# Optimization experiments

Measured on AMD Instinct MI355X. Metric: run time of the kernel, lower is better.

Reference implementation:

```python
import jax, jax.numpy as jnp
import numpy as np

EPS = 1e-5

def setup_inputs() -> dict:
    key = jax.random.key(0)
    ks = jax.random.split(key, 4)
    B, C, H, W = 32, 256, 32, 32
    x = jax.random.normal(ks[0], (B, C, H, W), dtype=jnp.float32)
    gamma = jnp.ones((C,), dtype=jnp.float32)
    beta = jnp.zeros((C,), dtype=jnp.float32)
    # torch nn.Linear init scale ~ 1/sqrt(fan_in)
    W_kqv = jax.random.normal(ks[1], (3 * C, C), dtype=jnp.float32) / np.sqrt(C)
    b_kqv = jnp.zeros((3 * C,), dtype=jnp.float32)
    W_proj = jax.random.normal(ks[2], (C, C), dtype=jnp.float32) / np.sqrt(C)
    b_proj = jnp.zeros((C,), dtype=jnp.float32)
    return {"x": x, "gamma": gamma, "beta": beta, "W_kqv": W_kqv,
            "b_kqv": b_kqv, "W_proj": W_proj, "b_proj": b_proj}

def reference(x, gamma, beta, W_kqv, b_kqv, W_proj, b_proj):
    B, C, H, W = x.shape
    scale = jnp.sqrt(jnp.asarray(C, dtype=x.dtype))
    # BatchNorm2d (training-mode batch statistics, biased variance, eps=1e-5)
    mean = jnp.mean(x, axis=(0, 2, 3), keepdims=True)
    var = jnp.var(x, axis=(0, 2, 3), keepdims=True)
    t = (x - mean) * jax.lax.rsqrt(var + EPS)
    t = t * gamma[None, :, None, None] + beta[None, :, None, None]
    # [B, C, H, W] -> [B, N, C] with N = H*W
    t = t.reshape(B, C, H * W).transpose(0, 2, 1)
    kqv = t @ W_kqv.T + b_kqv           # [B, N, 3C]
    q, k, v = jnp.split(kqv, 3, axis=-1)  # each [B, N, C]
    s = jnp.einsum('bnc,bmc->bnm', q, k) / scale  # [B, N, N]
    attn = jax.nn.softmax(s, axis=-1)
    o = jnp.einsum('bnm,bmc->bnc', attn, v)        # [B, N, C]
    o = o @ W_proj.T + b_proj
    o = o.transpose(0, 2, 1).reshape(B, C, H, W)
    return o + x
```

## Files before the change

kernel.cpp:

```cpp
#include <hip/hip_runtime.h>

typedef unsigned short u16;
typedef __attribute__((ext_vector_type(8))) short bf16x8;
typedef __attribute__((ext_vector_type(4))) float f32x4;

__device__ __forceinline__ float bf2f(u16 u) {
  union { unsigned u; float f; } c; c.u = ((unsigned)u) << 16; return c.f;
}
__device__ __forceinline__ u16 f2bf(float f) {
  union { float f; unsigned u; } c; c.f = f;
  unsigned u = c.u;
  return (u16)((u + 0x7FFFu + ((u >> 16) & 1u)) >> 16);
}
__device__ __forceinline__ void gld16(const void* g, void* l) {
  __builtin_amdgcn_global_load_lds(
      (__attribute__((address_space(1))) void*)g,
      (__attribute__((address_space(3))) void*)l, 16, 0, 0);
}

#define SYNCB() do { \
  asm volatile("s_waitcnt vmcnt(0) lgkmcnt(0)" ::: "memory"); \
  __builtin_amdgcn_s_barrier(); \
  __builtin_amdgcn_sched_barrier(0); \
} while (0)

#define BB 32
#define CC 256
#define NN 1024

__global__ __launch_bounds__(256) void convert_w_kernel(
    const float* __restrict__ Wk, const float* __restrict__ bk,
    const float* __restrict__ Wp, const float* __restrict__ bp,
    u16* __restrict__ Wkb, u16* __restrict__ bkb,
    u16* __restrict__ Wpb, u16* __restrict__ bpb)
{
  int b = blockIdx.x, t = threadIdx.x;
  const float* src; u16* dst; int idx, n;
  if (b < 768)       { src = Wk; dst = Wkb; idx = b * 256 + t;        n = 196608; }
  else if (b < 771)  { src = bk; dst = bkb; idx = (b - 768) * 256 + t; n = 768;   }
  else if (b < 1027) { src = Wp; dst = Wpb; idx = (b - 771) * 256 + t; n = 65536; }
  else               { src = bp; dst = bpb; idx = t;                  n = 256;    }
  if (idx < n) dst[idx] = f2bf(src[idx]);
}

__global__ __launch_bounds__(256) void bn_stats_kernel(
    const float* __restrict__ x, const float* __restrict__ gamma,
    const float* __restrict__ beta, float* __restrict__ scl, float* __restrict__ sft)
{
  int c = blockIdx.x;
  int tid = threadIdx.x;
  float s = 0.f, q = 0.f;
  for (int g = tid; g < 8192; g += 256) {
    int b = g >> 8;
    int n = (g & 255) * 4;
    float4 v = *reinterpret_cast<const float4*>(x + (((size_t)(b * CC + c)) << 10) + n);
    s += v.x + v.y + v.z + v.w;
    q += v.x * v.x + v.y * v.y + v.z * v.z + v.w * v.w;
  }
  __shared__ float rs[256], rq[256];
  rs[tid] = s; rq[tid] = q;
  __syncthreads();
  for (int off = 128; off > 0; off >>= 1) {
    if (tid < off) { rs[tid] += rs[tid + off]; rq[tid] += rq[tid + off]; }
    __syncthreads();
  }
  if (tid == 0) {
    float mean = rs[0] * (1.f / 32768.f);
    float var  = rq[0] * (1.f / 32768.f) - mean * mean;
    float rstd = rsqrtf(var + 1e-5f);
    float g = gamma[c] * rstd;
    scl[c] = g;
    sft[c] = beta[c] - mean * g;
  }
}

__global__ __launch_bounds__(256, 2) void qkv_fused_kernel(
    const float* __restrict__ x, const float* __restrict__ scl,
    const float* __restrict__ sft, const u16* __restrict__ Wkb,
    const u16* __restrict__ bkb, u16* __restrict__ qkout, u16* __restrict__ vt)
{
  __shared__ __align__(16) u16 As[128 * 32];
  __shared__ __align__(16) u16 Bs[256 * 32];
  int bid = blockIdx.x;
  int bx = bid & 255, by = bid >> 8;
  int b = bx >> 3, nsp0 = (bx & 7) * 128;
  int tid = threadIdx.x, lane = tid & 63, w = tid >> 6;
  int lq = lane & 15, quad = lane >> 4;
  int wm = (w >> 1) * 64, wn = (w & 1) * 128;
  int ar = lane >> 2, ac = (lane & 3) * 8;
  int rbB = w * 64;
  int nn = tid & 127, ci0 = (tid >> 7) * 16;

  const float* xb = x + (((size_t)(b * CC)) << 10) + nsp0 + nn;
  const u16* Bw = Wkb + (size_t)(by * 256) * 256;

  f32x4 zero = {0.f, 0.f, 0.f, 0.f};
  f32x4 acc[4][8];
  #pragma unroll
  for (int i = 0; i < 4; ++i)
    #pragma unroll
    for (int j = 0; j < 8; ++j) acc[i][j] = zero;

  int swz = (nn >> 1) & 3;
  int jj0 = ci0 >> 3;

  for (int k0 = 0; k0 < 256; k0 += 32) {
    __syncthreads();
    #pragma unroll
    for (int i = 0; i < 4; ++i)
      gld16(Bw + (size_t)(rbB + i * 16 + ar) * 256 + k0 + ac,
            &Bs[(rbB + i * 16) * 32]);
    float sv[16], hv[16];
    #pragma unroll
    for (int g = 0; g < 4; ++g) {
      float4 a = *reinterpret_cast<const float4*>(scl + k0 + ci0 + g * 4);
      float4 d = *reinterpret_cast<const float4*>(sft + k0 + ci0 + g * 4);
      sv[g * 4 + 0] = a.x; sv[g * 4 + 1] = a.y; sv[g * 4 + 2] = a.z; sv[g * 4 + 3] = a.w;
      hv[g * 4 + 0] = d.x; hv[g * 4 + 1] = d.y; hv[g * 4 + 2] = d.z; hv[g * 4 + 3] = d.w;
    }
    u16 av[16];
    #pragma unroll
    for (int i = 0; i < 16; ++i) {
      float v = xb[((size_t)(k0 + ci0 + i)) << 10];
      av[i] = f2bf(v * sv[i] + hv[i]);
    }
    bf16x8 p0, p1;
    #pragma unroll
    for (int i = 0; i < 8; ++i) { p0[i] = (short)av[i]; p1[i] = (short)av[i + 8]; }
    *reinterpret_cast<bf16x8*>(&As[nn * 32 + ((jj0 ^ swz) << 3)]) = p0;
    *reinterpret_cast<bf16x8*>(&As[nn * 32 + (((jj0 + 1) ^ swz) << 3)]) = p1;
    __syncthreads();

    bf16x8 af[4], bfr[8];
    #pragma unroll
    for (int i = 0; i < 4; ++i) {
      int r = wm + i * 16 + lq;
      af[i] = *reinterpret_cast<const bf16x8*>(
          &As[r * 32 + ((quad ^ ((r >> 1) & 3)) << 3)]);
    }
    #pragma unroll
    for (int j = 0; j < 8; ++j)
      bfr[j] = *reinterpret_cast<const bf16x8*>(
          &Bs[(wn + j * 16 + lq) * 32 + quad * 8]);
    #pragma unroll
    for (int i = 0; i < 4; ++i)
      #pragma unroll
      for (int j = 0; j < 8; ++j)
        acc[i][j] = __builtin_amdgcn_mfma_f32_16x16x32_bf16(af[i], bfr[j], acc[i][j], 0, 0, 0);
  }

  if (by < 2) {
    #pragma unroll
    for (int j = 0; j < 8; ++j) {
      int col = by * 256 + wn + j * 16 + lq;
      float bv = bf2f(bkb[col]);
      #pragma unroll
      for (int i = 0; i < 4; ++i) {
        int m = (b << 10) + nsp0 + wm + i * 16 + quad * 4;
        #pragma unroll
        for (int r = 0; r < 4; ++r)
          qkout[(size_t)(m + r) * 512 + col] = f2bf(acc[i][j][r] + bv);
      }
    }
  } else {
    #pragma unroll
    for (int j = 0; j < 8; ++j) {
      int col = wn + j * 16 + lq;
      float bv = bf2f(bkb[512 + col]);
      #pragma unroll
      for (int i = 0; i < 4; ++i) {
        int n = nsp0 + wm + i * 16 + quad * 4;
        ushort4 o;
        o.x = f2bf(acc[i][j][0] + bv);
        o.y = f2bf(acc[i][j][1] + bv);
        o.z = f2bf(acc[i][j][2] + bv);
        o.w = f2bf(acc[i][j][3] + bv);
        *reinterpret_cast<ushort4*>(&vt[(size_t)b * 262144 + (size_t)col * 1024 + n]) = o;
      }
    }
  }
}

__global__ __launch_bounds__(256) void gemm_nt_kernel(
    const u16* __restrict__ A, int lda, size_t sA,
    const u16* __restrict__ B, int ldb, size_t sB,
    u16* __restrict__ C, int ldc, size_t sC,
    int K, const u16* __restrict__ bias, float scale, int mode,
    const float* __restrict__ xres, float* __restrict__ outf)
{
  __shared__ u16 As[128 * 32];
  __shared__ u16 Bs[128 * 32];
  int tid = threadIdx.x;
  int m0 = blockIdx.x * 128, n0 = blockIdx.y * 128;
  const u16* Ab = A + (size_t)blockIdx.z * sA;
  const u16* Bb = B + (size_t)blockIdx.z * sB;
  u16* Cb = C + (size_t)blockIdx.z * sC;

  int lane = tid & 63, w = tid >> 6;
  int lq = lane & 15, quad = lane >> 4;
  int wm = (w >> 1) * 64, wn = (w & 1) * 64;
  int ar = lane >> 2, ac = (lane & 3) * 8;
  int rb = w * 32;

  f32x4 zero = {0.f, 0.f, 0.f, 0.f};
  f32x4 acc[4][4];
  #pragma unroll
  for (int i = 0; i < 4; ++i)
    #pragma unroll
    for (int j = 0; j < 4; ++j) acc[i][j] = zero;

  for (int k0 = 0; k0 < K; k0 += 32) {
    __syncthreads();
    gld16(Ab + (size_t)(m0 + rb +      ar) * lda + k0 + ac, &As[(rb     ) * 32]);
    gld16(Ab + (size_t)(m0 + rb + 16 + ar) * lda + k0 + ac, &As[(rb + 16) * 32]);
    gld16(Bb + (size_t)(n0 + rb +      ar) * ldb + k0 + ac, &Bs[(rb     ) * 32]);
    gld16(Bb + (size_t)(n0 + rb + 16 + ar) * ldb + k0 + ac, &Bs[(rb + 16) * 32]);
    __syncthreads();
    bf16x8 af[4], bfr[4];
    #pragma unroll
    for (int i = 0; i < 4; ++i) {
      af[i]  = *reinterpret_cast<const bf16x8*>(&As[(wm + i * 16 + lq) * 32 + quad * 8]);
      bfr[i] = *reinterpret_cast<const bf16x8*>(&Bs[(wn + i * 16 + lq) * 32 + quad * 8]);
    }
    #pragma unroll
    for (int i = 0; i < 4; ++i)
      #pragma unroll
      for (int j = 0; j < 4; ++j)
        acc[i][j] = __builtin_amdgcn_mfma_f32_16x16x32_bf16(af[i], bfr[j], acc[i][j], 0, 0, 0);
  }

  #pragma unroll
  for (int j = 0; j < 4; ++j) {
    int col = n0 + wn + j * 16 + lq;
    float bv = bias ? bf2f(bias[col]) : 0.f;
    #pragma unroll
    for (int i = 0; i < 4; ++i) {
      int rbase = m0 + wm + i * 16 + quad * 4;
      if (mode == 2) {
        int b = rbase >> 10, n = rbase & 1023;
        size_t idx = (((size_t)(b * CC + col)) << 10) + n;
        float4 xv = *reinterpret_cast<const float4*>(xres + idx);
        float4 o;
        o.x = acc[i][j][0] * scale + bv + xv.x;
        o.y = acc[i][j][1] * scale + bv + xv.y;
        o.z = acc[i][j][2] * scale + bv + xv.z;
        o.w = acc[i][j][3] * scale + bv + xv.w;
        *reinterpret_cast<float4*>(outf + idx) = o;
      } else {
        #pragma unroll
        for (int r = 0; r < 4; ++r)
          Cb[(size_t)(rbase + r) * ldc + col] = f2bf(acc[i][j][r] * scale + bv);
      }
    }
  }
}

__global__ __launch_bounds__(512, 2) void attn_kernel(
    const u16* __restrict__ qk,
    const u16* __restrict__ vt,
    u16* __restrict__ o)
{
  __shared__ __align__(16) u16 Ks[2][64 * 256];
  __shared__ __align__(16) u16 Vs[2][256 * 64];
  __shared__ __align__(16) u16 Ps[128 * 64];
  float* rs = (float*)Ps;

  int bid = blockIdx.x;
  int b  = (bid & 7) + 8 * ((bid >> 3) & 3);
  int qt = bid >> 5;
  int tid = threadIdx.x, lane = tid & 63, w = tid >> 6;
  int lq = lane & 15, hh = lane >> 4;
  int wr = w & 3;
  bool isQK = w < 4;

  const u16* qb = qk + ((size_t)b << 10) * 512;
  const u16* kb = qb + 256;
  const u16* vb = vt + ((size_t)b << 18);

  auto stageK = [&](int kt, int bufi) {
    #pragma unroll
    for (int i = 0; i < 4; ++i) {
      int slot = i * 512 + tid;
      int r = slot >> 5, c = slot & 31;
      gld16(kb + (size_t)(kt * 64 + r) * 512 + ((c ^ (r & 7)) << 3),
            &Ks[bufi][(i * 512 + (tid & 448)) * 8]);
    }
  };
  auto stageV = [&](int kt, int bufi) {
    #pragma unroll
    for (int i = 0; i < 4; ++i) {
      int slot = i * 512 + tid;
      int n = slot >> 3, c = slot & 7;
      gld16(vb + (size_t)(n << 10) + kt * 64 + ((c ^ (n & 7)) << 3),
            &Vs[bufi][(i * 512 + (tid & 448)) * 8]);
    }
  };

  f32x4 zero = {0.f, 0.f, 0.f, 0.f};

  stageK(0, 0);
  SYNCB();

  if (isQK) {
    int q0 = qt * 128 + wr * 32;
    bf16x8 qf[2][8];
    #pragma unroll
    for (int qi = 0; qi < 2; ++qi)
      #pragma unroll
      for (int kk = 0; kk < 8; ++kk)
        qf[qi][kk] = *reinterpret_cast<const bf16x8*>(
            qb + (size_t)(q0 + qi * 16 + lq) * 512 + kk * 32 + hh * 8);
    float runsum[2][4] = {{0.f, 0.f, 0.f, 0.f}, {0.f, 0.f, 0.f, 0.f}};

    #pragma unroll 1
    for (int p = 0; p <= 16; ++p) {
      if (p <= 15) stageV(p, p & 1);
      if (p <= 14) stageK(p + 1, (p + 1) & 1);
      u16 pbv[2][4][4];
      if (p <= 15) {
        const u16* Kc = Ks[p & 1];
        f32x4 sacc[2][4];
        #pragma unroll
        for (int qi = 0; qi < 2; ++qi)
          #pragma unroll
          for (int ni = 0; ni < 4; ++ni) sacc[qi][ni] = zero;
        #pragma unroll
        for (int kk = 0; kk < 8; ++kk) {
          bf16x8 kf[4];
          #pragma unroll
          for (int ni = 0; ni < 4; ++ni) {
            int r = ni * 16 + lq;
            kf[ni] = *reinterpret_cast<const bf16x8*>(
                &Kc[r * 256 + (((kk * 4 + hh) ^ (r & 7)) << 3)]);
          }
          __builtin_amdgcn_s_setprio(1);
          #pragma unroll
          for (int qi = 0; qi < 2; ++qi)
            #pragma unroll
            for (int ni = 0; ni < 4; ++ni)
              sacc[qi][ni] = __builtin_amdgcn_mfma_f32_16x16x32_bf16(
                  qf[qi][kk], kf[ni], sacc[qi][ni], 0, 0, 0);
          __builtin_amdgcn_s_setprio(0);
        }
        #pragma unroll
        for (int qi = 0; qi < 2; ++qi)
          #pragma unroll
          for (int ni = 0; ni < 4; ++ni)
            #pragma unroll
            for (int rr = 0; rr < 4; ++rr) {
              float pexp = __expf(sacc[qi][ni][rr] * 0.0625f);
              u16 pb = f2bf(pexp);
              runsum[qi][rr] += bf2f(pb);
              pbv[qi][ni][rr] = pb;
            }
      }
      SYNCB();
      if (p <= 15) {
        #pragma unroll
        for (int qi = 0; qi < 2; ++qi)
          #pragma unroll
          for (int ni = 0; ni < 4; ++ni)
            #pragma unroll
            for (int rr = 0; rr < 4; ++rr) {
              int q = wr * 32 + qi * 16 + hh * 4 + rr;
              int kcol = ni * 16 + lq;
              Ps[q * 64 + ((((kcol >> 3) ^ (q & 7)) << 3) | (kcol & 7))] =
                  pbv[qi][ni][rr];
            }
      }
      SYNCB();
    }

    #pragma unroll
    for (int qi = 0; qi < 2; ++qi)
      #pragma unroll
      for (int rr = 0; rr < 4; ++rr) {
        float s = runsum[qi][rr];
        s += __shfl_xor(s, 1, 64);
        s += __shfl_xor(s, 2, 64);
        s += __shfl_xor(s, 4, 64);
        s += __shfl_xor(s, 8, 64);
        if (lq == 0) rs[wr * 32 + qi * 16 + hh * 4 + rr] = 1.f / s;
      }
    SYNCB();
  } else {
    f32x4 oacc[8][4];
    #pragma unroll
    for (int qi = 0; qi < 8; ++qi)
      #pragma unroll
      for (int nj = 0; nj < 4; ++nj) oacc[qi][nj] = zero;

    #pragma unroll 1
    for (int p = 0; p <= 16; ++p) {
      if (p <= 15) stageV(p, p & 1);
      if (p <= 14) stageK(p + 1, (p + 1) & 1);
      if (p >= 1) {
        const u16* Vc = Vs[(p - 1) & 1];
        #pragma unroll
        for (int kk2 = 0; kk2 < 2; ++kk2) {
          bf16x8 pa[8];
          #pragma unroll
          for (int qi = 0; qi < 8; ++qi) {
            int r = qi * 16 + lq;
            pa[qi] = *reinterpret_cast<const bf16x8*>(
                &Ps[r * 64 + (((kk2 * 4 + hh) ^ (r & 7)) << 3)]);
          }
          bf16x8 vf[4];
          #pragma unroll
          for (int nj = 0; nj < 4; ++nj) {
            int n = wr * 64 + nj * 16 + lq;
            vf[nj] = *reinterpret_cast<const bf16x8*>(
                &Vc[n * 64 + (((kk2 * 4 + hh) ^ (n & 7)) << 3)]);
          }
          __builtin_amdgcn_s_setprio(1);
          #pragma unroll
          for (int qi = 0; qi < 8; ++qi)
            #pragma unroll
            for (int nj = 0; nj < 4; ++nj)
              oacc[qi][nj] = __builtin_amdgcn_mfma_f32_16x16x32_bf16(
                  pa[qi], vf[nj], oacc[qi][nj], 0, 0, 0);
          __builtin_amdgcn_s_setprio(0);
        }
      }
      SYNCB();
      SYNCB();
    }

    SYNCB();
    float rinv[8][4];
    #pragma unroll
    for (int qi = 0; qi < 8; ++qi)
      #pragma unroll
      for (int rr = 0; rr < 4; ++rr)
        rinv[qi][rr] = rs[qi * 16 + hh * 4 + rr];
    u16* ob = o + ((size_t)(b << 10) + qt * 128) * 256;
    #pragma unroll
    for (int qi = 0; qi < 8; ++qi)
      #pragma unroll
      for (int nj = 0; nj < 4; ++nj)
        #pragma unroll
        for (int rr = 0; rr < 4; ++rr)
          ob[(size_t)(qi * 16 + hh * 4 + rr) * 256 + wr * 64 + nj * 16 + lq] =
              f2bf(oacc[qi][nj][rr] * rinv[qi][rr]);
  }
}

extern "C" void kernel_launch(void* const* d_in, const int* in_sizes, int n_in,
                              void* d_out, int out_size, void* d_ws, size_t ws_size,
                              hipStream_t stream) {
  const float* x     = (const float*)d_in[0];
  const float* gamma = (const float*)d_in[1];
  const float* beta  = (const float*)d_in[2];
  const float* Wkqv  = (const float*)d_in[3];
  const float* bkqv  = (const float*)d_in[4];
  const float* Wproj = (const float*)d_in[5];
  const float* bproj = (const float*)d_in[6];
  float* out = (float*)d_out;

  char* ws = (char*)d_ws;
  float* scl    = (float*)ws;
  float* sft    = (float*)(ws + 1024);
  u16* Wkb = (u16*)(ws + 4096);
  u16* bkb = Wkb + 196608;
  u16* Wpb = bkb + 768;
  u16* bpb = Wpb + 65536;
  u16* qk   = (u16*)(ws + 1048576);
  u16* vt   = qk + (size_t)32768 * 512;
  u16* o_pv = vt + (size_t)32 * 256 * 1024;

  convert_w_kernel<<<dim3(1028), dim3(256), 0, stream>>>(
      Wkqv, bkqv, Wproj, bproj, Wkb, bkb, Wpb, bpb);
  bn_stats_kernel<<<dim3(256), dim3(256), 0, stream>>>(x, gamma, beta, scl, sft);
  qkv_fused_kernel<<<dim3(768), dim3(256), 0, stream>>>(
      x, scl, sft, Wkb, bkb, qk, vt);
  attn_kernel<<<dim3(256), dim3(512), 0, stream>>>(qk, vt, o_pv);
  gemm_nt_kernel<<<dim3(256, 2, 1), dim3(256), 0, stream>>>(
      o_pv, 256, 0, Wpb, 256, 0, nullptr, 0, 0, 256, bpb, 1.0f, 2, x, out);
}
```

Baseline: 203.8 us.

## Double-buffer QKV GEMM tiles and prefetch next x slice in registers

The fused BN+QKV projection kernel now double-buffers the A and B LDS tiles. It issues the global loads for the next K-slice (weights via global_load_lds, x values into registers) before the current slice's MFMAs, so memory latency overlaps compute. The BN scale/shift vectors are staged once in shared memory instead of being reloaded from global memory each iteration. MFMA sections are raised in priority with s_setprio. Per-block LDS and register usage go up, which could lower occupancy, and the hand-written vmcnt(20) wait count has to match the number of loads actually in flight.

After: 197.4 us. 1.03x faster.

```diff
diff --git a/kernel.cpp b/kernel.cpp
--- a/kernel.cpp
+++ b/kernel.cpp
@@ -79,8 +79,9 @@
     const float* __restrict__ sft, const u16* __restrict__ Wkb,
     const u16* __restrict__ bkb, u16* __restrict__ qkout, u16* __restrict__ vt)
 {
-  __shared__ __align__(16) u16 As[128 * 32];
-  __shared__ __align__(16) u16 Bs[256 * 32];
+  __shared__ __align__(16) u16 As[2][128 * 32];
+  __shared__ __align__(16) u16 Bs[2][256 * 32];
+  __shared__ __align__(16) float SS[512];
   int bid = blockIdx.x;
   int bx = bid & 255, by = bid >> 8;
   int b = bx >> 3, nsp0 = (bx & 7) * 128;
@@ -104,49 +105,87 @@
   int swz = (nn >> 1) & 3;
   int jj0 = ci0 >> 3;
 
-  for (int k0 = 0; k0 < 256; k0 += 32) {
-    __syncthreads();
-    #pragma unroll
-    for (int i = 0; i < 4; ++i)
-      gld16(Bw + (size_t)(rbB + i * 16 + ar) * 256 + k0 + ac,
-            &Bs[(rbB + i * 16) * 32]);
+  if (tid < 128) {
+    const float* src = (tid < 64) ? (scl + tid * 4) : (sft + (tid - 64) * 4);
+    float4 v = *reinterpret_cast<const float4*>(src);
+    *reinterpret_cast<float4*>(&SS[(tid < 64) ? tid * 4 : 256 + (tid - 64) * 4]) = v;
+  }
+  __syncthreads();
+
+  float xA[16], xB[16];
+  #pragma unroll
+  for (int i = 0; i < 4; ++i)
+    gld16(Bw + (size_t)(rbB + i * 16 + ar) * 256 + ac, &Bs[0][(rbB + i * 16) * 32]);
+  #pragma unroll
+  for (int i = 0; i < 16; ++i)
+    xA[i] = xb[((size_t)(ci0 + i)) << 10];
+
+  auto body = [&](int t, float (&xc)[16], float (&xn)[16]) {
+    int k0 = t * 32;
+    if (t < 7) {
+      int kn = k0 + 32;
+      #pragma unroll
+      for (int i = 0; i < 4; ++i)
+        gld16(Bw + (size_t)(rbB + i * 16 + ar) * 256 + kn + ac,
+              &Bs[(t + 1) & 1][(rbB + i * 16) * 32]);
+      #pragma unroll
+      for (int i = 0; i < 16; ++i)
+        xn[i] = xb[((size_t)(kn + ci0 + i)) << 10];
+    }
     float sv[16], hv[16];
     #pragma unroll
     for (int g = 0; g < 4; ++g) {
-      float4 a = *reinterpret_cast<const float4*>(scl + k0 + ci0 + g * 4);
-      float4 d = *reinterpret_cast<const float4*>(sft + k0 + ci0 + g * 4);
-      sv[g * 4 + 0] = a.x; sv[g * 4 + 1] = a.y; sv[g * 4 + 2] = a.z; sv[g * 4 + 3] = a.w;
-      hv[g * 4 + 0] = d.x; hv[g * 4 + 1] = d.y; hv[g * 4 + 2] = d.z; hv[g * 4 + 3] = d.w;
-    }
+      f32x4 a = *reinterpret_cast<const f32x4*>(&SS[k0 + ci0 + g * 4]);
+      f32x4 d = *reinterpret_cast<const f32x4*>(&SS[256 + k0 + ci0 + g * 4]);
+      sv[g * 4 + 0] = a[0]; sv[g * 4 + 1] = a[1]; sv[g * 4 + 2] = a[2]; sv[g * 4 + 3] = a[3];
+      hv[g * 4 + 0] = d[0]; hv[g * 4 + 1] = d[1]; hv[g * 4 + 2] = d[2]; hv[g * 4 + 3] = d[3];
+    }
+    if (t < 7) {
+      asm volatile("s_waitcnt vmcnt(20)" ::: "memory");
+    } else {
+      asm volatile("s_waitcnt vmcnt(0)" ::: "memory");
+    }
+    __builtin_amdgcn_sched_barrier(0);
     u16 av[16];
     #pragma unroll
-    for (int i = 0; i < 16; ++i) {
-      float v = xb[((size_t)(k0 + ci0 + i)) << 10];
-      av[i] = f2bf(v * sv[i] + hv[i]);
-    }
+    for (int i = 0; i < 16; ++i)
+      av[i] = f2bf(xc[i] * sv[i] + hv[i]);
     bf16x8 p0, p1;
     #pragma unroll
     for (int i = 0; i < 8; ++i) { p0[i] = (short)av[i]; p1[i] = (short)av[i + 8]; }
-    *reinterpret_cast<bf16x8*>(&As[nn * 32 + ((jj0 ^ swz) << 3)]) = p0;
-    *reinterpret_cast<bf16x8*>(&As[nn * 32 + (((jj0 + 1) ^ swz) << 3)]) = p1;
-    __syncthreads();
+    *reinterpret_cast<bf16x8*>(&As[t & 1][nn * 32 + ((jj0 ^ swz) << 3)]) = p0;
+    *reinterpret_cast<bf16x8*>(&As[t & 1][nn * 32 + (((jj0 + 1) ^ swz) << 3)]) = p1;
+    asm volatile("s_waitcnt lgkmcnt(0)" ::: "memory");
+    __builtin_amdgcn_s_barrier();
+    __builtin_amdgcn_sched_barrier(0);
 
     bf16x8 af[4], bfr[8];
     #pragma unroll
     for (int i = 0; i < 4; ++i) {
       int r = wm + i * 16 + lq;
       af[i] = *reinterpret_cast<const bf16x8*>(
-          &As[r * 32 + ((quad ^ ((r >> 1) & 3)) << 3)]);
+          &As[t & 1][r * 32 + ((quad ^ ((r >> 1) & 3)) << 3)]);
     }
     #pragma unroll
     for (int j = 0; j < 8; ++j)
       bfr[j] = *reinterpret_cast<const bf16x8*>(
-          &Bs[(wn + j * 16 + lq) * 32 + quad * 8]);
+          &Bs[t & 1][(wn + j * 16 + lq) * 32 + quad * 8]);
+    __builtin_amdgcn_s_setprio(1);
     #pragma unroll
     for (int i = 0; i < 4; ++i)
       #pragma unroll
       for (int j = 0; j < 8; ++j)
         acc[i][j] = __builtin_amdgcn_mfma_f32_16x16x32_bf16(af[i], bfr[j], acc[i][j], 0, 0, 0);
+    __builtin_amdgcn_s_setprio(0);
+    asm volatile("s_waitcnt lgkmcnt(0)" ::: "memory");
+    __builtin_amdgcn_s_barrier();
+    __builtin_amdgcn_sched_barrier(0);
+  };
+
+  #pragma unroll 1
+  for (int tt = 0; tt < 4; ++tt) {
+    body(2 * tt,     xA, xB);
+    body(2 * tt + 1, xB, xA);
   }
 
   if (by < 2) {
```
